# Performance work log

Hardware: AMD Instinct MI355X
Metric: run time of the kernel (lower is better)

The kernel has to match this reference:

```python
import jax, jax.numpy as jnp
import numpy as np

MAX_POS = float(2 ** 20)  # max_position_encoding_distance
B, C, S = 2, 1536, 16384
H, T, P = 768, 367, 128
NUM_ORG = 2


def _apply_rope(x, positions):
    # x: (B, P, T, H), positions: (B, P) int -> rotate pairs (first-half, second-half)
    half = x.shape[-1] // 2
    inv_freq = 1.0 / (MAX_POS ** (jnp.arange(half, dtype=jnp.float32) / half))  # (half,)
    ang = positions.astype(jnp.float32)[:, :, None, None] * inv_freq  # (B, P, 1, half)
    cos, sin = jnp.cos(ang), jnp.sin(ang)
    x1, x2 = x[..., :half], x[..., half:]
    return jnp.concatenate([x1 * cos - x2 * sin, x1 * sin + x2 * cos], axis=-1)


def _gather_affine_rope(logits, idx, params, organism_index):
    # logits: (B, H, S); idx: (B, P); params: (ORG, 2, T, H)
    bi = jnp.arange(logits.shape[0])[:, None]
    x = logits[bi, :, idx]  # (B, P, H)
    bp = params[organism_index]  # (B, 2, T, H)
    scale = bp[:, 0][:, None]   # (B, 1, T, H)
    offset = bp[:, 1][:, None]  # (B, 1, T, H)
    x = scale * x[:, :, None, :] + offset  # (B, P, T, H)
    return _apply_rope(x, idx)


def setup_inputs() -> dict:
    key = jax.random.key(0)
    ks = jax.random.split(key, 9)
    stdv = 1.0 / np.sqrt(C)
    return {
        'embeddings_1bp': jax.random.normal(ks[0], (B, C, S), jnp.float32),
        'conv_w': jax.random.normal(ks[1], (NUM_ORG, H, C), jnp.float32) * stdv,
        'conv_b': jax.random.normal(ks[2], (NUM_ORG, H), jnp.float32) * 0.02,
        'rope_pos_donor': jax.random.normal(ks[3], (NUM_ORG, 2, T, H), jnp.float32) * 0.05,
        'rope_pos_acceptor': jax.random.normal(ks[4], (NUM_ORG, 2, T, H), jnp.float32) * 0.05,
        'rope_neg_donor': jax.random.normal(ks[5], (NUM_ORG, 2, T, H), jnp.float32) * 0.05,
        'rope_neg_acceptor': jax.random.normal(ks[6], (NUM_ORG, 2, T, H), jnp.float32) * 0.05,
        'organism_index': jax.random.randint(ks[7], (B,), 0, NUM_ORG),
        'splice_site_positions': jax.random.randint(ks[8], (B, 4, P), 0, S),
    }


def reference(embeddings_1bp, conv_w, conv_b, rope_pos_donor, rope_pos_acceptor,
              rope_neg_donor, rope_neg_acceptor, organism_index, splice_site_positions):
    pos_d, pos_a = splice_site_positions[:, 0], splice_site_positions[:, 1]
    neg_d, neg_a = splice_site_positions[:, 2], splice_site_positions[:, 3]

    # organism-indexed 1x1 conv: (B,C,S) x (B,H,C) -> (B,H,S)
    w = conv_w[organism_index]
    b = conv_b[organism_index]
    logits = jnp.einsum('bcs,boc->bos', embeddings_1bp, w) + b[:, :, None]

    pdl = _gather_affine_rope(logits, pos_d, rope_pos_donor, organism_index)
    pal = _gather_affine_rope(logits, pos_a, rope_pos_acceptor, organism_index)
    ndl = _gather_affine_rope(logits, neg_d, rope_neg_donor, organism_index)
    nal = _gather_affine_rope(logits, neg_a, rope_neg_acceptor, organism_index)

    pos_counts = jax.nn.softplus(jnp.einsum('bdth,bath->bdat', pdl, pal))  # (B,P,P,T)
    neg_counts = jax.nn.softplus(jnp.einsum('bdth,bath->bdat', ndl, nal))

    pos_mask = (pos_d >= 0)[:, :, None] & (pos_a >= 0)[:, None, :]  # (B,P,P)
    neg_mask = (neg_d >= 0)[:, :, None] & (neg_a >= 0)[:, None, :]
    # tissue_mask: default num_tracks_per_organism -> all True
    tissue_mask = jnp.ones((B, T), dtype=bool)
    pos_mask = pos_mask[:, :, :, None] & tissue_mask[:, None, None, :]
    neg_mask = neg_mask[:, :, :, None] & tissue_mask[:, None, None, :]

    junction_mask = jnp.concatenate([pos_mask, neg_mask], axis=-1)  # (B,P,P,2T)
    pred_counts = jnp.concatenate([pos_counts, neg_counts], axis=-1)
    pred_counts = jnp.where(junction_mask, pred_counts, 0.0)
    return pred_counts, junction_mask
```

## Files before the change

### kernel.cpp

```cpp
#include <hip/hip_runtime.h>
#include <hip/hip_bf16.h>
#include <math.h>
#include <string.h>

#define B_    2
#define C_    1536
#define S_    16384
#define H_    768
#define T_    367
#define P_    128
#define HALF_ 384
#define TT_   734
#define NT2_  184
#define PRED_ELEMS 24051712

#define XHH_OFF  0
#define CSH_OFF  393216
#define INVF_OFF 786432
#define XCB_OFF  787200
#define W1WS_OFF 1573632

typedef short short8 __attribute__((ext_vector_type(8)));
typedef _Float16 f16x8 __attribute__((ext_vector_type(8)));
typedef _Float16 h2    __attribute__((ext_vector_type(2)));
typedef float f32x4  __attribute__((ext_vector_type(4)));

__device__ __forceinline__ unsigned int packbf2(float a, float b) {
    __hip_bfloat162 h = __float22bfloat162_rn(make_float2(a, b));
    unsigned int r; __builtin_memcpy(&r, &h, 4); return r;
}
__device__ __forceinline__ unsigned short packbf1(float a) {
    __hip_bfloat16 h = __float2bfloat16(a);
    unsigned short r; __builtin_memcpy(&r, &h, 2); return r;
}
__device__ __forceinline__ unsigned short f2h(float x) {
    _Float16 h = (_Float16)x;
    unsigned short r; __builtin_memcpy(&r, &h, 2); return r;
}
__device__ __forceinline__ h2 bch(unsigned int v) { h2 r; __builtin_memcpy(&r, &v, 4); return r; }
__device__ __forceinline__ unsigned int hcb(h2 v) { unsigned int r; __builtin_memcpy(&r, &v, 4); return r; }

__global__ void gather_cols(const float* __restrict__ emb,
                            const int* __restrict__ sp,
                            unsigned short* __restrict__ xcb) {
    int blk = blockIdx.x;
    int p = blk & 127;
    int g = (blk >> 7) & 3;
    int b = blk >> 9;
    int s = sp[(b * 4 + g) * P_ + p];
    const float* src = emb + (size_t)b * C_ * S_ + s;
    unsigned short* dst = xcb + ((size_t)(b * 4 + g) * P_ + p) * C_;
    for (int c = threadIdx.x; c < C_; c += blockDim.x)
        dst[c] = packbf1(src[(size_t)c * S_]);
}

__global__ __launch_bounds__(256) void logits_mfma(
    const unsigned short* __restrict__ xcb, const float* __restrict__ w,
    const float* __restrict__ bias, const int* __restrict__ org,
    unsigned short* __restrict__ xhh) {
    __shared__ __align__(16) unsigned short tX[64 * 64];
    __shared__ __align__(16) unsigned short tW[64 * 64];
    int mt = blockIdx.x;
    int nt = blockIdx.y;
    int o = org[mt >> 3];
    int r0 = mt * 64, h0 = nt * 64;
    int tid = threadIdx.x;
    int lane = tid & 63, wid = tid >> 6;
    int wrow = (wid >> 1) * 32, wcol = (wid & 1) * 32;
    int lr = lane & 15, lq = lane >> 4;
    int gr0 = (lq ^ (lr & 7)) * 8;

    f32x4 acc[2][2];
    #pragma unroll
    for (int i = 0; i < 2; ++i)
        #pragma unroll
        for (int j = 0; j < 2; ++j) acc[i][j] = (f32x4){0.f, 0.f, 0.f, 0.f};

    int srow = tid >> 2, sg = tid & 3;

    for (int kc = 0; kc < C_; kc += 64) {
        if (kc) __syncthreads();
        {
            const unsigned short* src = xcb + (size_t)(r0 + srow) * C_ + kc;
            unsigned short* drow = tX + srow * 64;
            #pragma unroll
            for (int i = 0; i < 2; ++i) {
                int g = sg + i * 4;
                uint4 v = *(const uint4*)(src + g * 8);
                *(uint4*)&drow[(g ^ (srow & 7)) * 8] = v;
            }
        }
        {
            const float* srcw = w + ((size_t)o * H_ + h0 + srow) * C_ + kc;
            unsigned short* drow = tW + srow * 64;
            #pragma unroll
            for (int i = 0; i < 2; ++i) {
                int g = sg + i * 4;
                float4 v0 = *(const float4*)(srcw + g * 8);
                float4 v1 = *(const float4*)(srcw + g * 8 + 4);
                uint4 pk;
                pk.x = packbf2(v0.x, v0.y); pk.y = packbf2(v0.z, v0.w);
                pk.z = packbf2(v1.x, v1.y); pk.w = packbf2(v1.z, v1.w);
                *(uint4*)&drow[(g ^ (srow & 7)) * 8] = pk;
            }
        }
        __syncthreads();
        #pragma unroll
        for (int kk = 0; kk < 64; kk += 32) {
            short8 af[2], bf2[2];
            #pragma unroll
            for (int fi = 0; fi < 2; ++fi)
                af[fi] = *(const short8*)&tX[(wrow + fi * 16 + lr) * 64 + (gr0 ^ kk)];
            #pragma unroll
            for (int fj = 0; fj < 2; ++fj)
                bf2[fj] = *(const short8*)&tW[(wcol + fj * 16 + lr) * 64 + (gr0 ^ kk)];
            #pragma unroll
            for (int fi = 0; fi < 2; ++fi)
                #pragma unroll
                for (int fj = 0; fj < 2; ++fj)
                    acc[fi][fj] = __builtin_amdgcn_mfma_f32_16x16x32_bf16(
                        af[fi], bf2[fj], acc[fi][fj], 0, 0, 0);
        }
    }
    #pragma unroll
    for (int fi = 0; fi < 2; ++fi)
        #pragma unroll
        for (int rr = 0; rr < 4; ++rr) {
            int r = r0 + wrow + fi * 16 + lq * 4 + rr;
            #pragma unroll
            for (int fj = 0; fj < 2; ++fj) {
                int h = h0 + wcol + fj * 16 + lr;
                int hj = (h < HALF_) ? h : (h - HALF_);
                int sel = (h < HALF_) ? 0 : 1;
                xhh[(size_t)r * H_ + (hj >> 2) * 8 + sel * 4 + (hj & 3)] =
                    f2h(acc[fi][fj][rr] + bias[o * H_ + h]);
            }
        }
}

__global__ void init_invf(double* __restrict__ invf) {
    int j = threadIdx.x;
    if (j < HALF_) invf[j] = exp2(-20.0 * (double)j / 384.0);
}

__global__ void rope_table(const int* __restrict__ sp,
                           const double* __restrict__ invf,
                           unsigned short* __restrict__ csh) {
    int e = blockIdx.x * blockDim.x + threadIdx.x;
    if (e >= B_ * 4 * P_ * HALF_) return;
    int j = e % HALF_;
    int r = e / HALF_;
    int s = sp[r];
    const double TWO_PI = 6.283185307179586476925286766559;
    double ang = (double)s * invf[j];
    double k = rint(ang * (1.0 / TWO_PI));
    float fr = (float)(ang - k * TWO_PI);
    float sv, cv;
    __sincosf(fr, &sv, &cv);
    int base = r * H_ + (j >> 2) * 8 + (j & 3);
    csh[base]     = f2h(cv);
    csh[base + 4] = f2h(sv);
}

#define BUILD4(cof, xv, cAh, cBh, sAh, sBh, dst)                               \
    {                                                                          \
        uint4 sc = *(const uint4*)((cof) + kb);                                \
        uint4 of = *(const uint4*)((cof) + 768 + kb);                          \
        h2 u1a = __builtin_elementwise_fma(bch(sc.x), bch((xv).x), bch(of.x)); \
        h2 u1b = __builtin_elementwise_fma(bch(sc.y), bch((xv).y), bch(of.y)); \
        h2 u2a = __builtin_elementwise_fma(bch(sc.z), bch((xv).z), bch(of.z)); \
        h2 u2b = __builtin_elementwise_fma(bch(sc.w), bch((xv).w), bch(of.w)); \
        uint4 wv;                                                              \
        wv.x = hcb(__builtin_elementwise_fma(u1a, (cAh), -(u2a * (sAh))));     \
        wv.y = hcb(__builtin_elementwise_fma(u1b, (cBh), -(u2b * (sBh))));     \
        wv.z = hcb(__builtin_elementwise_fma(u1a, (sAh), u2a * (cAh)));        \
        wv.w = hcb(__builtin_elementwise_fma(u1b, (sBh), u2b * (cBh)));        \
        *(uint4*)&(dst) = wv;                                                  \
    }

__global__ __launch_bounds__(1024, 4) void junction_mfma(
    const unsigned short* __restrict__ xhh, const unsigned short* __restrict__ csh,
    const float* __restrict__ rpd, const float* __restrict__ rpa,
    const float* __restrict__ rnd, const float* __restrict__ rna,
    const int* __restrict__ org, const int* __restrict__ sp,
    unsigned short* __restrict__ w1) {
    __shared__ __align__(16) unsigned short smem[65536];
    __shared__ __align__(16) unsigned short scofh[6144];
    __shared__ int vD[P_], vA[P_];

    int nwg = gridDim.x;
    int orig = blockIdx.x;
    int xcd = orig & 7;
    int q = nwg >> 3, r8 = nwg & 7;
    int blk = (xcd < r8 ? xcd * (q + 1) : r8 * (q + 1) + (xcd - r8) * q) + (orig >> 3);

    int tp = blk % NT2_;
    int sign = (blk / NT2_) & 1;
    int b = blk / (2 * NT2_);
    int o = org[b];
    int t0 = 2 * tp, t1 = t0 + 1;
    int t1ok = (t1 < T_);
    int t1c = t1ok ? t1 : t0;
    int gd = sign * 2, ga = sign * 2 + 1;
    const float* pd = sign ? rnd : rpd;
    const float* pa = sign ? rna : rpa;
    int tid = threadIdx.x;

    for (int e = tid; e < 6144; e += 1024) {
        int tsel_ = e / 3072;
        int rem = e - tsel_ * 3072;
        int side = rem / 1536;
        int rem2 = rem - side * 1536;
        int arr = rem2 / 768;
        int e2 = rem2 - arr * 768;
        int tt = tsel_ ? t1c : t0;
        const float* base = (side ? pa : pd) + ((size_t)(o * 2 + arr) * T_ + tt) * H_;
        int hj = (e2 < HALF_) ? e2 : (e2 - HALF_);
        int sel = (e2 < HALF_) ? 0 : 1;
        int pos = (hj >> 2) * 8 + sel * 4 + (hj & 3);
        scofh[((tsel_ * 2 + side) * 2 + arr) * 768 + pos] = f2h(base[e2]);
    }
    if (tid < P_) {
        vD[tid] = sp[(b * 4 + gd) * P_ + tid] >= 0;
        vA[tid] = sp[(b * 4 + ga) * P_ + tid] >= 0;
    }
    const unsigned short* xdh = xhh + ((size_t)(b * 4 + gd) * P_) * H_;
    const unsigned short* xah = xhh + ((size_t)(b * 4 + ga) * P_) * H_;
    const unsigned short* cdh = csh + ((size_t)(b * 4 + gd) * P_) * H_;
    const unsigned short* cah = csh + ((size_t)(b * 4 + ga) * P_) * H_;

    int lane = tid & 63, wid = tid >> 6;
    int tsel = wid >> 3;
    int w8 = wid & 7;
    int wrow = (w8 >> 2) * 64, wcol = (w8 & 3) * 32;
    int lr = lane & 15, lq = lane >> 4;
    int gr0 = (lq ^ (lr & 7)) * 8;

    f32x4 acc[4][2];
    #pragma unroll
    for (int i = 0; i < 4; ++i)
        #pragma unroll
        for (int j = 0; j < 2; ++j) acc[i][j] = (f32x4){0.f, 0.f, 0.f, 0.f};

    int prow = tid >> 3, gran = tid & 7;
    int sw = prow * 64 + ((gran ^ (prow & 7)) << 3);
    const unsigned short* xd_t = xdh + prow * H_ + gran * 8;
    const unsigned short* cd_t = cdh + prow * H_ + gran * 8;
    const unsigned short* xa_t = xah + prow * H_ + gran * 8;
    const unsigned short* ca_t = cah + prow * H_ + gran * 8;

    uint4 pxd = *(const uint4*)xd_t;
    uint4 pcd = *(const uint4*)cd_t;
    uint4 pxa = *(const uint4*)xa_t;
    uint4 pca = *(const uint4*)ca_t;

    __syncthreads();

    for (int ch = 0; ch < 12; ++ch) {
        unsigned short* bufb = smem + (ch & 1) * 32768;
        int kb = (ch * 8 + gran) * 8;

        {
            h2 cA = bch(pcd.x), cB = bch(pcd.y), sA = bch(pcd.z), sB = bch(pcd.w);
            BUILD4(scofh,        pxd, cA, cB, sA, sB, bufb[sw]);
            BUILD4(scofh + 3072, pxd, cA, cB, sA, sB, bufb[16384 + sw]);
        }
        {
            h2 cA = bch(pca.x), cB = bch(pca.y), sA = bch(pca.z), sB = bch(pca.w);
            BUILD4(scofh + 1536, pxa, cA, cB, sA, sB, bufb[8192 + sw]);
            BUILD4(scofh + 4608, pxa, cA, cB, sA, sB, bufb[24576 + sw]);
        }
        if (ch < 11) {
            int o2 = (ch + 1) * 64;
            pxd = *(const uint4*)(xd_t + o2);
            pcd = *(const uint4*)(cd_t + o2);
            pxa = *(const uint4*)(xa_t + o2);
            pca = *(const uint4*)(ca_t + o2);
        }
        __syncthreads();

        __builtin_amdgcn_s_setprio(1);
        {
            const unsigned short* tD = bufb + tsel * 16384;
            const unsigned short* tA = tD + 8192;
            #pragma unroll
            for (int kk = 0; kk < 64; kk += 32) {
                f16x8 af[4], bf2[2];
                #pragma unroll
                for (int fi = 0; fi < 4; ++fi)
                    af[fi] = *(const f16x8*)&tD[(wrow + fi * 16 + lr) * 64 + (gr0 ^ kk)];
                #pragma unroll
                for (int fj = 0; fj < 2; ++fj)
                    bf2[fj] = *(const f16x8*)&tA[(wcol + fj * 16 + lr) * 64 + (gr0 ^ kk)];
                #pragma unroll
                for (int fi = 0; fi < 4; ++fi)
                    #pragma unroll
                    for (int fj = 0; fj < 2; ++fj)
                        acc[fi][fj] = __builtin_amdgcn_mfma_f32_16x16x32_f16(
                            af[fi], bf2[fj], acc[fi][fj], 0, 0, 0);
            }
        }
        __builtin_amdgcn_s_setprio(0);
    }

    #pragma unroll
    for (int fi = 0; fi < 4; ++fi) {
        #pragma unroll
        for (int rr = 0; rr < 4; ++rr) {
            int d = wrow + fi * 16 + lq * 4 + rr;
            int vd = vD[d];
            #pragma unroll
            for (int fj = 0; fj < 2; ++fj) {
                int a = wcol + fj * 16 + lr;
                float x = acc[fi][fj][rr];
                float v = 0.0f;
                if (vd && vA[a]) v = (x > 15.0f) ? x : __logf(1.0f + __expf(x));
                smem[tsel * 16384 + d * P_ + a] = packbf1(v);
            }
        }
    }
    __syncthreads();
    const uint4* s4 = (const uint4*)smem;
    uint4* d40 = (uint4*)(w1 + (size_t)((b * 2 + sign) * T_ + t0) * (P_ * P_));
    for (int i = tid; i < 2048; i += 1024) d40[i] = s4[i];
    if (t1ok) {
        uint4* d41 = (uint4*)(w1 + (size_t)((b * 2 + sign) * T_ + t1) * (P_ * P_));
        for (int i = tid; i < 2048; i += 1024) d41[i] = s4[2048 + i];
    }
}

__global__ __launch_bounds__(256) void finalize_ws(const __hip_bfloat16* __restrict__ w1,
                                                   const int* __restrict__ sp,
                                                   float* __restrict__ pred,
                                                   float* __restrict__ mask) {
    __shared__ float tile[64 * 129];
    __shared__ float mval[P_];
    int blk = blockIdx.x;
    int tt = blk % 6;
    int d = (blk / 6) % P_;
    int bs = blk / (6 * P_);
    int b = bs >> 1, sign = bs & 1;
    int t0 = tt * 64;
    int tcnt = min(64, T_ - t0);
    int tid = threadIdx.x;

    const __hip_bfloat16* src = w1 + (size_t)bs * T_ * P_ * P_ + (size_t)d * P_;
    for (int e = tid; e < tcnt * P_; e += 256) {
        int i = e >> 7, a = e & 127;
        tile[i * 129 + a] = __bfloat162float(src[(size_t)(t0 + i) * P_ * P_ + a]);
    }
    if (tid < P_) {
        bool vd = sp[(b * 4 + sign * 2) * P_ + d] >= 0;
        bool va = sp[(b * 4 + sign * 2 + 1) * P_ + tid] >= 0;
        mval[tid] = (vd && va) ? 1.0f : 0.0f;
    }
    __syncthreads();
    size_t obase = ((size_t)(b * P_ + d) * P_) * TT_ + sign * T_ + t0;
    float* dstp = pred + obase;
    float* dstm = mask + obase;
    for (int e = tid; e < P_ * 64; e += 256) {
        int a = e >> 6, ii = e & 63;
        if (ii < tcnt) {
            dstp[(size_t)a * TT_ + ii] = tile[ii * 129 + a];
            dstm[(size_t)a * TT_ + ii] = mval[a];
        }
    }
}

__global__ __launch_bounds__(256) void transpose_out(const __hip_bfloat16* __restrict__ w1,
                                                     float* __restrict__ pred) {
    __shared__ float tile[64 * 129];
    int blk = blockIdx.x;
    int tt = blk % 6;
    int d = (blk / 6) % P_;
    int bs = blk / (6 * P_);
    int b = bs >> 1, sign = bs & 1;
    int t0 = tt * 64;
    int tcnt = min(64, T_ - t0);
    int tid = threadIdx.x;

    const __hip_bfloat16* src = w1 + (size_t)bs * T_ * P_ * P_ + (size_t)d * P_;
    for (int e = tid; e < tcnt * P_; e += 256) {
        int i = e >> 7, a = e & 127;
        tile[i * 129 + a] = __bfloat162float(src[(size_t)(t0 + i) * P_ * P_ + a]);
    }
    __syncthreads();
    float* dst = pred + ((size_t)(b * P_ + d) * P_) * TT_ + sign * T_ + t0;
    for (int e = tid; e < P_ * 64; e += 256) {
        int a = e >> 6, ii = e & 63;
        if (ii < tcnt) dst[(size_t)a * TT_ + ii] = tile[ii * 129 + a];
    }
}

__global__ void mask_fill(const int* __restrict__ sp, float* __restrict__ mask) {
    int blk = blockIdx.x;
    int a = blk & 127;
    int d = (blk >> 7) & 127;
    int b = blk >> 14;
    bool vp = (sp[(b * 4 + 0) * P_ + d] >= 0) && (sp[(b * 4 + 1) * P_ + a] >= 0);
    bool vn = (sp[(b * 4 + 2) * P_ + d] >= 0) && (sp[(b * 4 + 3) * P_ + a] >= 0);
    float* dst = mask + (size_t)blk * TT_;
    for (int st = threadIdx.x; st < TT_; st += blockDim.x)
        dst[st] = (st < T_ ? vp : vn) ? 1.0f : 0.0f;
}

extern "C" void kernel_launch(void* const* d_in, const int* in_sizes, int n_in,
                              void* d_out, int out_size, void* d_ws, size_t ws_size,
                              hipStream_t stream) {
    const float* emb  = (const float*)d_in[0];
    const float* w    = (const float*)d_in[1];
    const float* bias = (const float*)d_in[2];
    const float* rpd  = (const float*)d_in[3];
    const float* rpa  = (const float*)d_in[4];
    const float* rnd  = (const float*)d_in[5];
    const float* rna  = (const float*)d_in[6];
    const int*   org  = (const int*)d_in[7];
    const int*   sp   = (const int*)d_in[8];

    float* out = (float*)d_out;
    float* ws  = (float*)d_ws;
    unsigned short* xhh = (unsigned short*)(ws + XHH_OFF);
    unsigned short* csh = (unsigned short*)(ws + CSH_OFF);
    double* invf = (double*)(ws + INVF_OFF);
    unsigned short* xcb = (unsigned short*)(ws + XCB_OFF);
    float* pred  = out;
    float* maskp = out + PRED_ELEMS;

    size_t w1_bytes = (size_t)4 * T_ * P_ * P_ * 2;
    size_t need = (size_t)W1WS_OFF * 4 + w1_bytes;
    bool ws_ok = (ws_size >= need);
    unsigned short* w1 = ws_ok ? (unsigned short*)(ws + W1WS_OFF)
                               : (unsigned short*)maskp;

    init_invf<<<1, 384, 0, stream>>>(invf);
    gather_cols<<<1024, 256, 0, stream>>>(emb, sp, xcb);
    rope_table<<<1536, 256, 0, stream>>>(sp, invf, csh);
    dim3 gl(16, 12);
    logits_mfma<<<gl, 256, 0, stream>>>(xcb, w, bias, org, xhh);
    junction_mfma<<<2 * 2 * NT2_, 1024, 0, stream>>>(xhh, csh, rpd, rpa, rnd, rna, org, sp, w1);
    if (ws_ok) {
        finalize_ws<<<2 * 2 * P_ * 6, 256, 0, stream>>>((const __hip_bfloat16*)w1, sp, pred, maskp);
    } else {
        transpose_out<<<2 * 2 * P_ * 6, 256, 0, stream>>>((const __hip_bfloat16*)w1, pred);
        mask_fill<<<32768, 256, 0, stream>>>(sp, maskp);
    }
}
```

Measured before the change: 230.9 us.

## Halve K-chunk size to shrink shared memory and interleave donor/acceptor rows

```diff
diff --git a/kernel.cpp b/kernel.cpp
--- a/kernel.cpp
+++ b/kernel.cpp
@@ -178,13 +178,13 @@
         *(uint4*)&(dst) = wv;                                                  \
     }
 
-__global__ __launch_bounds__(1024, 4) void junction_mfma(
+__global__ __launch_bounds__(1024, 8) void junction_mfma(
     const unsigned short* __restrict__ xhh, const unsigned short* __restrict__ csh,
     const float* __restrict__ rpd, const float* __restrict__ rpa,
     const float* __restrict__ rnd, const float* __restrict__ rna,
     const int* __restrict__ org, const int* __restrict__ sp,
     unsigned short* __restrict__ w1) {
-    __shared__ __align__(16) unsigned short smem[65536];
+    __shared__ __align__(16) unsigned short smem[32768];
     __shared__ __align__(16) unsigned short scofh[6144];
     __shared__ int vD[P_], vA[P_];
 
@@ -209,16 +209,16 @@
     for (int e = tid; e < 6144; e += 1024) {
         int tsel_ = e / 3072;
         int rem = e - tsel_ * 3072;
-        int side = rem / 1536;
-        int rem2 = rem - side * 1536;
+        int side_ = rem / 1536;
+        int rem2 = rem - side_ * 1536;
         int arr = rem2 / 768;
         int e2 = rem2 - arr * 768;
         int tt = tsel_ ? t1c : t0;
-        const float* base = (side ? pa : pd) + ((size_t)(o * 2 + arr) * T_ + tt) * H_;
+        const float* base = (side_ ? pa : pd) + ((size_t)(o * 2 + arr) * T_ + tt) * H_;
         int hj = (e2 < HALF_) ? e2 : (e2 - HALF_);
         int sel = (e2 < HALF_) ? 0 : 1;
         int pos = (hj >> 2) * 8 + sel * 4 + (hj & 3);
-        scofh[((tsel_ * 2 + side) * 2 + arr) * 768 + pos] = f2h(base[e2]);
+        scofh[((tsel_ * 2 + side_) * 2 + arr) * 768 + pos] = f2h(base[e2]);
     }
     if (tid < P_) {
         vD[tid] = sp[(b * 4 + gd) * P_ + tid] >= 0;
@@ -234,7 +234,7 @@
     int w8 = wid & 7;
     int wrow = (w8 >> 2) * 64, wcol = (w8 & 3) * 32;
     int lr = lane & 15, lq = lane >> 4;
-    int gr0 = (lq ^ (lr & 7)) * 8;
+    int grA = (lq ^ (lr & 7)) << 3;
 
     f32x4 acc[4][2];
     #pragma unroll
@@ -242,67 +242,56 @@
         #pragma unroll
         for (int j = 0; j < 2; ++j) acc[i][j] = (f32x4){0.f, 0.f, 0.f, 0.f};
 
-    int prow = tid >> 3, gran = tid & 7;
-    int sw = prow * 64 + ((gran ^ (prow & 7)) << 3);
-    const unsigned short* xd_t = xdh + prow * H_ + gran * 8;
-    const unsigned short* cd_t = cdh + prow * H_ + gran * 8;
-    const unsigned short* xa_t = xah + prow * H_ + gran * 8;
-    const unsigned short* ca_t = cah + prow * H_ + gran * 8;
-
-    uint4 pxd = *(const uint4*)xd_t;
-    uint4 pcd = *(const uint4*)cd_t;
-    uint4 pxa = *(const uint4*)xa_t;
-    uint4 pca = *(const uint4*)ca_t;
+    int prow = tid >> 3, g = tid & 7;
+    int side = g >> 2, gc = g & 3;
+    const unsigned short* x_t = (side ? xah : xdh) + prow * H_ + gc * 8;
+    const unsigned short* c_t = (side ? cah : cdh) + prow * H_ + gc * 8;
+    int sw = prow * 64 + ((g ^ (prow & 7)) << 3);
+    const unsigned short* cof0 = scofh + side * 1536;
+    const unsigned short* cof1 = scofh + 3072 + side * 1536;
+
+    uint4 pxv = *(const uint4*)x_t;
+    uint4 pcv = *(const uint4*)c_t;
 
     __syncthreads();
 
-    for (int ch = 0; ch < 12; ++ch) {
-        unsigned short* bufb = smem + (ch & 1) * 32768;
-        int kb = (ch * 8 + gran) * 8;
+    for (int ch = 0; ch < 24; ++ch) {
+        unsigned short* bufb = smem + (ch & 1) * 16384;
+        int kb = (ch * 4 + gc) * 8;
 
         {
-            h2 cA = bch(pcd.x), cB = bch(pcd.y), sA = bch(pcd.z), sB = bch(pcd.w);
-            BUILD4(scofh,        pxd, cA, cB, sA, sB, bufb[sw]);
-            BUILD4(scofh + 3072, pxd, cA, cB, sA, sB, bufb[16384 + sw]);
-        }
-        {
-            h2 cA = bch(pca.x), cB = bch(pca.y), sA = bch(pca.z), sB = bch(pca.w);
-            BUILD4(scofh + 1536, pxa, cA, cB, sA, sB, bufb[8192 + sw]);
-            BUILD4(scofh + 4608, pxa, cA, cB, sA, sB, bufb[24576 + sw]);
-        }
-        if (ch < 11) {
-            int o2 = (ch + 1) * 64;
-            pxd = *(const uint4*)(xd_t + o2);
-            pcd = *(const uint4*)(cd_t + o2);
-            pxa = *(const uint4*)(xa_t + o2);
-            pca = *(const uint4*)(ca_t + o2);
+            h2 cA = bch(pcv.x), cB = bch(pcv.y), sA = bch(pcv.z), sB = bch(pcv.w);
+            BUILD4(cof0, pxv, cA, cB, sA, sB, bufb[sw]);
+            BUILD4(cof1, pxv, cA, cB, sA, sB, bufb[8192 + sw]);
+        }
+        if (ch < 23) {
+            int o2 = (ch + 1) * 32;
+            pxv = *(const uint4*)(x_t + o2);
+            pcv = *(const uint4*)(c_t + o2);
         }
         __syncthreads();
 
         __builtin_amdgcn_s_setprio(1);
         {
-            const unsigned short* tD = bufb + tsel * 16384;
-            const unsigned short* tA = tD + 8192;
-            #pragma unroll
-            for (int kk = 0; kk < 64; kk += 32) {
-                f16x8 af[4], bf2[2];
-                #pragma unroll
-                for (int fi = 0; fi < 4; ++fi)
-                    af[fi] = *(const f16x8*)&tD[(wrow + fi * 16 + lr) * 64 + (gr0 ^ kk)];
+            const unsigned short* tb = bufb + tsel * 8192;
+            f16x8 af[4], bf2[2];
+            #pragma unroll
+            for (int fi = 0; fi < 4; ++fi)
+                af[fi] = *(const f16x8*)&tb[(wrow + fi * 16 + lr) * 64 + grA];
+            #pragma unroll
+            for (int fj = 0; fj < 2; ++fj)
+                bf2[fj] = *(const f16x8*)&tb[(wcol + fj * 16 + lr) * 64 + (grA ^ 32)];
+            #pragma unroll
+            for (int fi = 0; fi < 4; ++fi)
                 #pragma unroll
                 for (int fj = 0; fj < 2; ++fj)
-                    bf2[fj] = *(const f16x8*)&tA[(wcol + fj * 16 + lr) * 64 + (gr0 ^ kk)];
-                #pragma unroll
-                for (int fi = 0; fi < 4; ++fi)
-                    #pragma unroll
-                    for (int fj = 0; fj < 2; ++fj)
-                        acc[fi][fj] = __builtin_amdgcn_mfma_f32_16x16x32_f16(
-                            af[fi], bf2[fj], acc[fi][fj], 0, 0, 0);
-            }
+                    acc[fi][fj] = __builtin_amdgcn_mfma_f32_16x16x32_f16(
+                        af[fi], bf2[fj], acc[fi][fj], 0, 0, 0);
         }
         __builtin_amdgcn_s_setprio(0);
     }
 
+    __syncthreads();
     #pragma unroll
     for (int fi = 0; fi < 4; ++fi) {
         #pragma unroll
```

Result: slower. 270.9 us (+17.3%).
